# Kernel optimization log

Measured on AMD Instinct MI355X. Metric: run time of the kernel, lower is better.

## Reference

```python
import jax, jax.numpy as jnp
import numpy as np


def setup_inputs() -> dict:
    key = jax.random.key(0)
    k1, k2, k3 = jax.random.split(key, 3)
    B, S, D_IN, D_OUT = 2, 2048, 4096, 4096
    x = jax.random.normal(k1, (B, S, D_IN), dtype=jnp.float32)
    # int8 quantized weight (stored as int32 container, values in int8 range)
    weight = jax.random.randint(k2, (D_OUT, D_IN), 0, 127, dtype=jnp.int32)
    weight_scaler = jax.random.uniform(k3, (D_OUT,), dtype=jnp.float32)
    return {"x": x, "weight": weight, "weight_scaler": weight_scaler}


def reference(x, weight, weight_scaler):
    # Dequantize per-output-channel: w_fp = int8_weight * scaler[:, None]
    w = weight.astype(jnp.float32) * weight_scaler[:, None]  # [O, I]
    # F.linear: x @ w.T
    return jnp.einsum("bsi,oi->bso", x, w)
```

## Files before the change

### kernel.cpp

```cpp
#include <hip/hip_runtime.h>

typedef int i32x4 __attribute__((ext_vector_type(4)));

#define AS1 __attribute__((address_space(1)))
#define AS3 __attribute__((address_space(3)))

__global__ __launch_bounds__(256) void quant_kernel(
    const float4* __restrict__ x, const int4* __restrict__ w,
    signed char* __restrict__ xq, signed char* __restrict__ wq,
    float* __restrict__ sx, int M, int Kq) {
  const int tid = threadIdx.x;
  if ((int)blockIdx.x < M) {
    const int r = blockIdx.x;
    float4 v[4];
    #pragma unroll
    for (int j = 0; j < 4; ++j) v[j] = x[(size_t)r * 1024 + j * 256 + tid];
    float m = 0.f;
    #pragma unroll
    for (int j = 0; j < 4; ++j)
      m = fmaxf(m, fmaxf(fmaxf(fabsf(v[j].x), fabsf(v[j].y)),
                         fmaxf(fabsf(v[j].z), fabsf(v[j].w))));
    #pragma unroll
    for (int off = 1; off < 64; off <<= 1) m = fmaxf(m, __shfl_xor(m, off));
    __shared__ float wmax[4];
    if ((tid & 63) == 0) wmax[tid >> 6] = m;
    __syncthreads();
    m = fmaxf(fmaxf(wmax[0], wmax[1]), fmaxf(wmax[2], wmax[3]));
    const float inv = (m > 0.f) ? 127.0f / m : 0.f;
    if (tid == 0) sx[r] = m * (1.0f / 127.0f);
    int* out = (int*)xq;
    #pragma unroll
    for (int j = 0; j < 4; ++j) {
      const int q0 = __float2int_rn(v[j].x * inv) & 255;
      const int q1 = __float2int_rn(v[j].y * inv) & 255;
      const int q2 = __float2int_rn(v[j].z * inv) & 255;
      const int q3 = __float2int_rn(v[j].w * inv) & 255;
      out[(size_t)r * 1024 + j * 256 + tid] = q0 | (q1 << 8) | (q2 << 16) | (q3 << 24);
    }
  } else {
    const int b = blockIdx.x - M;
    int4 v[4];
    #pragma unroll
    for (int j = 0; j < 4; ++j) v[j] = w[(size_t)b * 1024 + j * 256 + tid];
    int* out = (int*)wq;
    #pragma unroll
    for (int j = 0; j < 4; ++j)
      out[(size_t)b * 1024 + j * 256 + tid] =
          (v[j].x & 255) | ((v[j].y & 255) << 8) | ((v[j].z & 255) << 16) | ((v[j].w & 255) << 24);
  }
}

__global__ __launch_bounds__(256, 2) void gemm_i8_kernel(
    const signed char* __restrict__ A,
    const signed char* __restrict__ B,
    const float* __restrict__ sx,
    const float* __restrict__ scaler,
    float* __restrict__ C,
    int M, int N, int K)
{
  __shared__ signed char sA[3][256 * 64];
  __shared__ signed char sB[3][128 * 64];

  const int tid  = threadIdx.x;
  const int wave = tid >> 6;
  const int lane = tid & 63;

  const int lin = (int)(blockIdx.y * gridDim.x + blockIdx.x);
  const int swz = (lin & 7) * 64 + (lin >> 3);
  const int bxs = swz & 31;
  const int bys = swz >> 5;
  const int bm = bys << 8;
  const int bn = bxs << 7;

  const int wm = (wave >> 1) << 7;
  const int wn = (wave & 1) << 6;
  const int l15  = lane & 15;
  const int quad = lane >> 4;

  const int srow = tid >> 2;
  const int kg = (tid & 3) ^ ((srow >> 1) & 3);
  const signed char* ga = A + (size_t)(bm + srow) * K + kg * 16;
  const signed char* gb = B + (size_t)(bn + srow) * K + kg * 16;
  const size_t rstep = (size_t)64 * K;
  const int ldst = tid * 16;

  const int pk   = (quad ^ ((l15 >> 1) & 3)) << 4;
  const int aoff = (wm + l15) * 64 + pk;
  const int boff = (wn + l15) * 64 + pk;

  i32x4 acc[8][4] = {};

#define STAGE(tt, sb) do { const size_t ko_ = (size_t)(tt) * 64;             \
    __builtin_amdgcn_global_load_lds((AS1 void*)(ga + ko_),             (AS3 void*)(&sA[sb][ldst]),         16, 0, 0); \
    __builtin_amdgcn_global_load_lds((AS1 void*)(ga + ko_ + rstep),     (AS3 void*)(&sA[sb][4096 + ldst]),  16, 0, 0); \
    __builtin_amdgcn_global_load_lds((AS1 void*)(ga + ko_ + 2 * rstep), (AS3 void*)(&sA[sb][8192 + ldst]),  16, 0, 0); \
    __builtin_amdgcn_global_load_lds((AS1 void*)(ga + ko_ + 3 * rstep), (AS3 void*)(&sA[sb][12288 + ldst]), 16, 0, 0); \
    __builtin_amdgcn_global_load_lds((AS1 void*)(gb + ko_),             (AS3 void*)(&sB[sb][ldst]),         16, 0, 0); \
    __builtin_amdgcn_global_load_lds((AS1 void*)(gb + ko_ + rstep),     (AS3 void*)(&sB[sb][4096 + ldst]),  16, 0, 0); } while (0)

  const int nt = K >> 6;

  STAGE(0, 0); STAGE(1, 1);
  asm volatile("s_waitcnt vmcnt(6)" ::: "memory");
  __builtin_amdgcn_s_barrier();
  __builtin_amdgcn_sched_barrier(0);

  int br = 0;
  int bs = 2;
  for (int t = 0; t < nt; ++t) {
    const signed char* la = sA[br];
    const signed char* lb = sB[br];

    if (t < nt - 2) STAGE(t + 2, bs);

    i32x4 av[8], bv[4];
    #pragma unroll
    for (int ni = 0; ni < 4; ++ni) bv[ni] = *(const i32x4*)&lb[boff + ni * 1024];
    #pragma unroll
    for (int mi = 0; mi < 8; ++mi) av[mi] = *(const i32x4*)&la[aoff + mi * 1024];

    __builtin_amdgcn_s_setprio(1);
    #pragma unroll
    for (int mi = 0; mi < 8; ++mi)
      #pragma unroll
      for (int ni = 0; ni < 4; ++ni)
        acc[mi][ni] = __builtin_amdgcn_mfma_i32_16x16x64_i8(av[mi], bv[ni], acc[mi][ni], 0, 0, 0);
    __builtin_amdgcn_s_setprio(0);

    if (t < nt - 2)        asm volatile("s_waitcnt vmcnt(6)" ::: "memory");
    else if (t == nt - 2)  asm volatile("s_waitcnt vmcnt(0)" ::: "memory");
    if (t < nt - 1) {
      __builtin_amdgcn_s_barrier();
      __builtin_amdgcn_sched_barrier(0);
    }
    br = (br == 2) ? 0 : br + 1;
    bs = (bs == 2) ? 0 : bs + 1;
  }
#undef STAGE

  #pragma unroll
  for (int mi = 0; mi < 8; ++mi) {
    const int gm0 = bm + wm + mi * 16 + quad * 4;
    float sr[4];
    #pragma unroll
    for (int r = 0; r < 4; ++r) sr[r] = sx[gm0 + r];
    #pragma unroll
    for (int ni = 0; ni < 4; ++ni) {
      const int gn = bn + wn + ni * 16 + l15;
      const float sc = scaler[gn];
      #pragma unroll
      for (int r = 0; r < 4; ++r)
        C[(size_t)(gm0 + r) * N + gn] = (float)acc[mi][ni][r] * sr[r] * sc;
    }
  }
}

extern "C" void kernel_launch(void* const* d_in, const int* in_sizes, int n_in,
                              void* d_out, int out_size, void* d_ws, size_t ws_size,
                              hipStream_t stream) {
  const float* x  = (const float*)d_in[0];
  const int*   w  = (const int*)d_in[1];
  const float* sc = (const float*)d_in[2];
  float* out = (float*)d_out;

  const int N = in_sizes[2];
  const int K = in_sizes[1] / N;
  const int M = in_sizes[0] / K;

  signed char* Aq = (signed char*)d_ws;
  signed char* Bq = Aq + (size_t)M * K;
  float* sx = (float*)(Bq + (size_t)N * K);

  const int wBlocks = (N * K) / (256 * 16);
  quant_kernel<<<M + wBlocks, 256, 0, stream>>>(
      (const float4*)x, (const int4*)w, Aq, Bq, sx, M, K / 16);

  dim3 grid(N / 128, M / 256);
  gemm_i8_kernel<<<grid, 256, 0, stream>>>(Aq, Bq, sx, sc, out, M, N, K);
}
```

Measured before the change: 240.6 us.

## Load B fragments directly from global into registers, bypassing LDS

The B (weight) tile no longer goes through LDS. Each wave now loads its own B MFMA fragments straight from global memory into registers, one K-step ahead, using register double-buffering. This removes the LDS traffic and space for B, which lowers LDS pressure. In exchange, each of the two M-row waves sharing an N column fetches the same B data separately, and the vmcnt accounting gets harder. The waitcnt values, which mix A's async LDS loads with B's register loads, may also not order correctly.

```diff
diff --git a/kernel.cpp b/kernel.cpp
--- a/kernel.cpp
+++ b/kernel.cpp
@@ -59,7 +59,6 @@
     int M, int N, int K)
 {
   __shared__ signed char sA[3][256 * 64];
-  __shared__ signed char sB[3][128 * 64];
 
   const int tid  = threadIdx.x;
   const int wave = tid >> 6;
@@ -67,10 +66,8 @@
 
   const int lin = (int)(blockIdx.y * gridDim.x + blockIdx.x);
   const int swz = (lin & 7) * 64 + (lin >> 3);
-  const int bxs = swz & 31;
-  const int bys = swz >> 5;
-  const int bm = bys << 8;
-  const int bn = bxs << 7;
+  const int bm = (swz >> 5) << 8;
+  const int bn = (swz & 31) << 7;
 
   const int wm = (wave >> 1) << 7;
   const int wn = (wave & 1) << 6;
@@ -80,28 +77,30 @@
   const int srow = tid >> 2;
   const int kg = (tid & 3) ^ ((srow >> 1) & 3);
   const signed char* ga = A + (size_t)(bm + srow) * K + kg * 16;
-  const signed char* gb = B + (size_t)(bn + srow) * K + kg * 16;
   const size_t rstep = (size_t)64 * K;
   const int ldst = tid * 16;
 
   const int pk   = (quad ^ ((l15 >> 1) & 3)) << 4;
   const int aoff = (wm + l15) * 64 + pk;
-  const int boff = (wn + l15) * 64 + pk;
+
+  const signed char* gB = B + (size_t)(bn + wn + l15) * K + quad * 16;
+  const size_t nstep = (size_t)16 * K;
 
   i32x4 acc[8][4] = {};
+  i32x4 bcur[4], bnext[4];
 
-#define STAGE(tt, sb) do { const size_t ko_ = (size_t)(tt) * 64;             \
+#define STAGE_A(tt, sb) do { const size_t ko_ = (size_t)(tt) * 64;           \
     __builtin_amdgcn_global_load_lds((AS1 void*)(ga + ko_),             (AS3 void*)(&sA[sb][ldst]),         16, 0, 0); \
     __builtin_amdgcn_global_load_lds((AS1 void*)(ga + ko_ + rstep),     (AS3 void*)(&sA[sb][4096 + ldst]),  16, 0, 0); \
     __builtin_amdgcn_global_load_lds((AS1 void*)(ga + ko_ + 2 * rstep), (AS3 void*)(&sA[sb][8192 + ldst]),  16, 0, 0); \
-    __builtin_amdgcn_global_load_lds((AS1 void*)(ga + ko_ + 3 * rstep), (AS3 void*)(&sA[sb][12288 + ldst]), 16, 0, 0); \
-    __builtin_amdgcn_global_load_lds((AS1 void*)(gb + ko_),             (AS3 void*)(&sB[sb][ldst]),         16, 0, 0); \
-    __builtin_amdgcn_global_load_lds((AS1 void*)(gb + ko_ + rstep),     (AS3 void*)(&sB[sb][4096 + ldst]),  16, 0, 0); } while (0)
+    __builtin_amdgcn_global_load_lds((AS1 void*)(ga + ko_ + 3 * rstep), (AS3 void*)(&sA[sb][12288 + ldst]), 16, 0, 0); } while (0)
 
   const int nt = K >> 6;
 
-  STAGE(0, 0); STAGE(1, 1);
-  asm volatile("s_waitcnt vmcnt(6)" ::: "memory");
+  STAGE_A(0, 0); STAGE_A(1, 1);
+  #pragma unroll
+  for (int ni = 0; ni < 4; ++ni) bnext[ni] = *(const i32x4*)(gB + ni * nstep);
+  asm volatile("s_waitcnt vmcnt(8)" ::: "memory");
   __builtin_amdgcn_s_barrier();
   __builtin_amdgcn_sched_barrier(0);
 
@@ -109,13 +108,17 @@
   int bs = 2;
   for (int t = 0; t < nt; ++t) {
     const signed char* la = sA[br];
-    const signed char* lb = sB[br];
 
-    if (t < nt - 2) STAGE(t + 2, bs);
+    #pragma unroll
+    for (int ni = 0; ni < 4; ++ni) bcur[ni] = bnext[ni];
+    if (t < nt - 1) {
+      #pragma unroll
+      for (int ni = 0; ni < 4; ++ni)
+        bnext[ni] = *(const i32x4*)(gB + ni * nstep + (size_t)(t + 1) * 64);
+    }
+    if (t < nt - 2) STAGE_A(t + 2, bs);
 
-    i32x4 av[8], bv[4];
-    #pragma unroll
-    for (int ni = 0; ni < 4; ++ni) bv[ni] = *(const i32x4*)&lb[boff + ni * 1024];
+    i32x4 av[8];
     #pragma unroll
     for (int mi = 0; mi < 8; ++mi) av[mi] = *(const i32x4*)&la[aoff + mi * 1024];
 
@@ -124,10 +127,10 @@
     for (int mi = 0; mi < 8; ++mi)
       #pragma unroll
       for (int ni = 0; ni < 4; ++ni)
-        acc[mi][ni] = __builtin_amdgcn_mfma_i32_16x16x64_i8(av[mi], bv[ni], acc[mi][ni], 0, 0, 0);
+        acc[mi][ni] = __builtin_amdgcn_mfma_i32_16x16x64_i8(av[mi], bcur[ni], acc[mi][ni], 0, 0, 0);
     __builtin_amdgcn_s_setprio(0);
 
-    if (t < nt - 2)        asm volatile("s_waitcnt vmcnt(6)" ::: "memory");
+    if (t < nt - 2)        asm volatile("s_waitcnt vmcnt(4)" ::: "memory");
     else if (t == nt - 2)  asm volatile("s_waitcnt vmcnt(0)" ::: "memory");
     if (t < nt - 1) {
       __builtin_amdgcn_s_barrier();
@@ -136,7 +139,7 @@
     br = (br == 2) ? 0 : br + 1;
     bs = (bs == 2) ? 0 : bs + 1;
   }
-#undef STAGE
+#undef STAGE_A
 
   #pragma unroll
   for (int mi = 0; mi < 8; ++mi) {
```

New measurement: 255.2 us. 6.1% more time.
